# Optimization experiments

Measured on AMD Instinct MI355X. Metric: run time of the kernel, lower is better.

## Reference

```python
import jax, jax.numpy as jnp
import numpy as np
from jax import lax

B, CIN, H, W = 16, 256, 64, 64
DP = 512          # displace_planes
COUT = 256        # outplanes
NUM_OFFSET = 64   # displace_planes // BIND_CHAN(8)
K = 5             # DPOOL_SIZE (odd)
EPS = float(np.finfo(np.float32).eps)
BN_EPS = 1e-5
EXP_CLAMP = 88.722835


def conv1x1(x, w, b):
    # x: [B,C,H,W], w: [O,C], b: [O]
    return jnp.einsum('bchw,oc->bohw', x, w) + b[None, :, None, None]


def batchnorm(x, gamma, beta):
    m = x.mean(axis=(0, 2, 3))
    v = x.var(axis=(0, 2, 3))
    inv = lax.rsqrt(v + BN_EPS)
    return (x - m[None, :, None, None]) * (inv * gamma)[None, :, None, None] + beta[None, :, None, None]


def dynamic_pool(x, sigma):
    # per-channel Gaussian depthwise conv in exp space, back to log space
    r = (jnp.arange(K) - K // 2).astype(jnp.float32)
    dissq = r[:, None] ** 2 + r[None, :] ** 2                     # [K,K]
    kern = jnp.exp(-(dissq / 2.0)[None] / (sigma ** 2 + EPS)[:, None, None])  # [C,K,K]
    kern = kern / kern.sum(axis=(1, 2), keepdims=True)
    expx = jnp.exp(jnp.minimum(x, EXP_CLAMP))
    out = lax.conv_general_dilated(
        expx, kern[:, None],                                      # rhs [C,1,K,K]
        window_strides=(1, 1), padding=[(K // 2, K // 2)] * 2,
        dimension_numbers=('NCHW', 'OIHW', 'NCHW'),
        feature_group_count=DP)
    return jnp.log(out + EPS)


def displace(feat, offsets):
    # feat: [B,C,H,W]; offsets: [NUM_OFFSET,2] (dy,dx), each bound to C//NUM_OFFSET channels.
    # Per-channel uniform bilinear shift with zero padding outside the map.
    Bn, C, Hn, Wn = feat.shape
    chan = C // NUM_OFFSET
    dy = jnp.repeat(offsets[:, 0], chan)  # [C]
    dx = jnp.repeat(offsets[:, 1], chan)
    y0 = jnp.floor(dy); x0 = jnp.floor(dx)
    fy = dy - y0; fx = dx - x0            # fractional parts (diff. wrt offsets)
    y0i = y0.astype(jnp.int32); x0i = x0.astype(jnp.int32)
    rows = jnp.arange(Hn); cols = jnp.arange(Wn)

    def one_chan(img, y0c, x0c, fyc, fxc):
        # img: [B,H,W]; shift is separable per row/col since offset is uniform
        def shifted(oy, ox):
            ry = rows + y0c + oy
            rx = cols + x0c + ox
            my = (ry >= 0) & (ry < Hn)
            mx = (rx >= 0) & (rx < Wn)
            g = img[:, jnp.clip(ry, 0, Hn - 1), :][:, :, jnp.clip(rx, 0, Wn - 1)]
            return g * (my[:, None] & mx[None, :]).astype(img.dtype)[None]
        return ((1 - fyc) * (1 - fxc) * shifted(0, 0)
                + (1 - fyc) * fxc * shifted(0, 1)
                + fyc * (1 - fxc) * shifted(1, 0)
                + fyc * fxc * shifted(1, 1))

    return jax.vmap(one_chan, in_axes=(1, 0, 0, 0, 0), out_axes=1)(feat, y0i, x0i, fy, fx)


def attention(x, w, b, gamma, beta):
    a = conv1x1(x, w, b)
    a = batchnorm(a, gamma, beta)
    a = jax.nn.softplus(a)
    # SpaceNormalization: normalize over spatial dims
    return a / a.sum(axis=(2, 3), keepdims=True)


def setup_inputs() -> dict:
    key = jax.random.key(0)
    ks = jax.random.split(key, 6)
    return {
        'x': jax.random.normal(ks[0], (B, CIN, H, W), jnp.float32),
        'pre_w': jax.random.normal(ks[1], (DP, CIN), jnp.float32) / np.sqrt(CIN),
        'pre_b': jnp.zeros((DP,), jnp.float32),
        'sigma': jnp.full((DP,), K / 2 / 2, jnp.float32),
        'offsets': jax.random.normal(ks[2], (NUM_OFFSET, 2), jnp.float32) * 3.0,
        'atten_w': jax.random.normal(ks[3], (DP, CIN), jnp.float32) / np.sqrt(CIN),
        'atten_b': jnp.zeros((DP,), jnp.float32),
        'atten_gamma': jnp.ones((DP,), jnp.float32),
        'atten_beta': jnp.zeros((DP,), jnp.float32),
        'post_w': jax.random.normal(ks[4], (COUT, DP), jnp.float32) / np.sqrt(DP),
        'post_b': jnp.zeros((COUT,), jnp.float32),
        'bn_gamma': jnp.ones((COUT,), jnp.float32),
        'bn_beta': jnp.zeros((COUT,), jnp.float32),
    }


def reference(x, pre_w, pre_b, sigma, offsets, atten_w, atten_b, atten_gamma,
              atten_beta, post_w, post_b, bn_gamma, bn_beta):
    out_pre = conv1x1(x, pre_w, pre_b)                 # [B,DP,H,W]
    out_pre = dynamic_pool(out_pre, sigma)
    out_dis = displace(out_pre, offsets)
    out_atten = attention(x, atten_w, atten_b, atten_gamma, atten_beta)
    out_post = conv1x1(out_atten * out_dis, post_w, post_b)  # [B,COUT,H,W]
    out_skip = x + out_post                            # inplanes==outplanes, stride=1
    return jax.nn.relu(batchnorm(out_skip, bn_gamma, bn_beta))
```

## Files before the change

### kernel.cpp

```cpp
#include <hip/hip_runtime.h>
#include <cmath>

#define NB   16
#define CINC 256
#define DPC  512
#define COUTC 256
#define HWS  4096
#define EPSF 1.1920928955078125e-07f
#define BN_EPS 1e-5f
#define EXP_CLAMP 88.722835f
#define SW 80

typedef unsigned int uint32;
typedef unsigned short ushort;
typedef __bf16 bf16x8 __attribute__((ext_vector_type(8)));
typedef float f32x4 __attribute__((ext_vector_type(4)));
typedef unsigned short ushort8 __attribute__((ext_vector_type(8)));

__device__ inline ushort f2bf(float f) {
    uint32 u = __builtin_bit_cast(uint32, f);
    u += 0x7fffu + ((u >> 16) & 1u);
    return (ushort)(u >> 16);
}
__device__ inline float bf2f(ushort u) {
    return __builtin_bit_cast(float, (uint32)u << 16);
}
__device__ inline float softplus_fast(float v) {
    return fmaxf(v, 0.f) + __logf(1.f + __expf(-fabsf(v)));
}
__device__ __forceinline__ void gload16(const void* g, void* l) {
    __builtin_amdgcn_global_load_lds(
        (__attribute__((address_space(1))) void*)g,
        (__attribute__((address_space(3))) void*)l, 16, 0, 0);
}

template<int OTOT, int KTOT, bool BF16_OUT, bool ADD_SKIP>
__global__ __launch_bounds__(256) void mfma_gemm_k(
    const ushort* __restrict__ A, const ushort* __restrict__ BT,
    const float* __restrict__ bias1, const float* __restrict__ bias2,
    const float* __restrict__ skip, void* __restrict__ outv) {
    const int hw0 = blockIdx.x * 128;
    const int o0  = blockIdx.y * 128;
    const int b   = blockIdx.z;
    __shared__ ushort As[128 * 32];
    __shared__ ushort Bs[128 * 32];
    const int tid  = threadIdx.x;
    const int lane = tid & 63;
    const int w    = tid >> 6;
    const int wm0  = (w >> 1) * 64;
    const int wn0  = (w & 1) * 64;

    f32x4 acc[4][4] = {};

    const ushort* Ab = A + (size_t)o0 * KTOT;
    const ushort* Bb = BT + ((size_t)b * HWS + hw0) * KTOT;
    const int rsub  = lane >> 2;
    const int ksubp = ((lane & 3) ^ ((lane >> 3) & 3)) * 8;

    for (int step = 0; step < KTOT / 32; ++step) {
        const int k0 = step * 32;
#pragma unroll
        for (int i = 0; i < 2; ++i) {
            const int row = w * 32 + i * 16 + rsub;
            gload16(Ab + (size_t)row * KTOT + k0 + ksubp, &As[(w * 32 + i * 16) * 32]);
            gload16(Bb + (size_t)row * KTOT + k0 + ksubp, &Bs[(w * 32 + i * 16) * 32]);
        }
        __syncthreads();
        bf16x8 af[4], bfr[4];
#pragma unroll
        for (int mi = 0; mi < 4; ++mi) {
            int row = wm0 + mi * 16 + (lane & 15);
            int sl = (lane >> 4) ^ ((row >> 1) & 3);
            af[mi] = *reinterpret_cast<const bf16x8*>(As + row * 32 + sl * 8);
        }
#pragma unroll
        for (int ni = 0; ni < 4; ++ni) {
            int row = wn0 + ni * 16 + (lane & 15);
            int sl = (lane >> 4) ^ ((row >> 1) & 3);
            bfr[ni] = *reinterpret_cast<const bf16x8*>(Bs + row * 32 + sl * 8);
        }
#pragma unroll
        for (int mi = 0; mi < 4; ++mi)
#pragma unroll
            for (int ni = 0; ni < 4; ++ni)
                acc[mi][ni] = __builtin_amdgcn_mfma_f32_16x16x32_bf16(af[mi], bfr[ni], acc[mi][ni], 0, 0, 0);
        __syncthreads();
    }

#pragma unroll
    for (int mi = 0; mi < 4; ++mi) {
#pragma unroll
        for (int r = 0; r < 4; ++r) {
            int o = o0 + wm0 + mi * 16 + ((lane >> 4) << 2) + r;
            float bi = (o < 512) ? bias1[o] : bias2[o - 512];
            size_t base = ((size_t)b * OTOT + o) * HWS + hw0 + wn0 + (lane & 15);
            if constexpr (BF16_OUT) {
                ushort* outp = (ushort*)outv;
#pragma unroll
                for (int ni = 0; ni < 4; ++ni)
                    outp[base + ni * 16] = f2bf(acc[mi][ni][r] + bi);
            } else {
                float* outp = (float*)outv;
#pragma unroll
                for (int ni = 0; ni < 4; ++ni) {
                    float v = acc[mi][ni][r] + bi;
                    if constexpr (ADD_SKIP) v += skip[base + ni * 16];
                    outp[base + ni * 16] = v;
                }
            }
        }
    }
}

__global__ __launch_bounds__(256) void castT_k(const float* __restrict__ x,
                                               ushort* __restrict__ xT) {
    const int b = blockIdx.z, c0 = blockIdx.y * 64, hw0 = blockIdx.x * 64;
    __shared__ float tile[64][65];
    const int tid = threadIdx.x;
#pragma unroll
    for (int r = 0; r < 16; ++r) {
        int cl = r * 4 + (tid >> 6), hwl = tid & 63;
        tile[cl][hwl] = x[((size_t)b * CINC + c0 + cl) * HWS + hw0 + hwl];
    }
    __syncthreads();
#pragma unroll
    for (int r = 0; r < 16; ++r) {
        int hwl = r * 4 + (tid >> 6), cl = tid & 63;
        xT[((size_t)b * HWS + hw0 + hwl) * CINC + c0 + cl] = f2bf(tile[cl][hwl]);
    }
}

__global__ __launch_bounds__(256) void cast_k(const float* __restrict__ in,
                                              ushort* __restrict__ out, int n) {
    int i = (blockIdx.x * 256 + threadIdx.x) * 4;
    if (i < n) {
        float4 v = *reinterpret_cast<const float4*>(in + i);
        out[i + 0] = f2bf(v.x); out[i + 1] = f2bf(v.y);
        out[i + 2] = f2bf(v.z); out[i + 3] = f2bf(v.w);
    }
}

__global__ __launch_bounds__(256) void pooldisp_k(ushort* __restrict__ dp,
                                                  const float* __restrict__ sigma,
                                                  const float* __restrict__ offsets) {
    const int bc = blockIdx.x;
    const int b = bc >> 9, c = bc & 511;
    __shared__ ushort ex[68 * SW];
    __shared__ ushort tmp[68 * SW];
    const int tid = threadIdx.x;
    ushort* ip = dp + ((size_t)b * 1024 + c) * HWS;

    float s = sigma[c];
    float inv = 0.5f / (s * s + EPSF);
    float g0 = __expf(-4.f * inv), g1 = __expf(-1.f * inv);
    float gs = g0 + g1 + 1.f + g1 + g0;
    float rnorm = 1.f / (gs * gs);

    if (tid < 168) {
        int row, colc;
        if (tid < 40) {
            row = (tid < 20) ? (tid / 10) : (66 + (tid - 20) / 10);
            colc = (tid % 10) * 8;
        } else {
            int k = tid - 40;
            row = 2 + (k >> 1);
            colc = (k & 1) ? 72 : 0;
        }
        ushort8 z = {0, 0, 0, 0, 0, 0, 0, 0};
        *reinterpret_cast<ushort8*>(&ex[row * SW + colc]) = z;
    }
#pragma unroll
    for (int t = 0; t < 2; ++t) {
        int p = (tid + t * 256) * 8;
        int h = p >> 6, w = p & 63;
        ushort8 v = *reinterpret_cast<const ushort8*>(ip + p);
        ushort8 e;
#pragma unroll
        for (int q = 0; q < 8; ++q)
            e[q] = f2bf(__expf(fminf(bf2f(v[q]), EXP_CLAMP)));
        *reinterpret_cast<ushort8*>(&ex[(h + 2) * SW + 8 + w]) = e;
    }
    __syncthreads();

    for (int t = 0; t < 3; ++t) {
        int task = tid + t * 256;
        if (task < 544) {
            int r = task >> 3, wgc = (task & 7) * 8;
            ushort8 c0 = *reinterpret_cast<const ushort8*>(&ex[r * SW + wgc]);
            ushort8 c1 = *reinterpret_cast<const ushort8*>(&ex[r * SW + wgc + 8]);
            ushort8 c2 = *reinterpret_cast<const ushort8*>(&ex[r * SW + wgc + 16]);
            float P[24];
#pragma unroll
            for (int q = 0; q < 8; ++q) {
                P[q] = bf2f(c0[q]); P[8 + q] = bf2f(c1[q]); P[16 + q] = bf2f(c2[q]);
            }
            ushort8 o;
#pragma unroll
            for (int j = 0; j < 8; ++j)
                o[j] = f2bf(g0 * (P[6 + j] + P[10 + j]) + g1 * (P[7 + j] + P[9 + j]) + P[8 + j]);
            *reinterpret_cast<ushort8*>(&tmp[r * SW + wgc + 8]) = o;
        }
    }
    __syncthreads();

#pragma unroll
    for (int t = 0; t < 2; ++t) {
        int task = tid + t * 256;
        int h = task >> 3, wgc = (task & 7) * 8;
        ushort8 t0 = *reinterpret_cast<const ushort8*>(&tmp[(h + 0) * SW + wgc + 8]);
        ushort8 t1 = *reinterpret_cast<const ushort8*>(&tmp[(h + 1) * SW + wgc + 8]);
        ushort8 t2 = *reinterpret_cast<const ushort8*>(&tmp[(h + 2) * SW + wgc + 8]);
        ushort8 t3 = *reinterpret_cast<const ushort8*>(&tmp[(h + 3) * SW + wgc + 8]);
        ushort8 t4 = *reinterpret_cast<const ushort8*>(&tmp[(h + 4) * SW + wgc + 8]);
        ushort8 o;
#pragma unroll
        for (int j = 0; j < 8; ++j) {
            float v = g0 * (bf2f(t0[j]) + bf2f(t4[j]))
                    + g1 * (bf2f(t1[j]) + bf2f(t3[j])) + bf2f(t2[j]);
            o[j] = f2bf(__logf(v * rnorm + EPSF));
        }
        *reinterpret_cast<ushort8*>(&ex[(h + 2) * SW + 8 + wgc]) = o;
    }
    __syncthreads();

    int oi = c >> 3;
    float dy = offsets[oi * 2 + 0];
    float dx = offsets[oi * 2 + 1];
    float y0f = floorf(dy), x0f = floorf(dx);
    float fy = dy - y0f, fx = dx - x0f;
    int y0 = (int)y0f, x0 = (int)x0f;
    float w00 = (1.f - fy) * (1.f - fx), w01 = (1.f - fy) * fx;
    float w10 = fy * (1.f - fx),         w11 = fy * fx;
#pragma unroll
    for (int t = 0; t < 2; ++t) {
        int p = (tid + t * 256) * 8;
        int h = p >> 6, w = p & 63;
        int ry0 = h + y0, ry1 = ry0 + 1;
        bool my0 = (ry0 >= 0) & (ry0 < 64);
        bool my1 = (ry1 >= 0) & (ry1 < 64);
        ushort8 ov;
#pragma unroll
        for (int q = 0; q < 8; ++q) {
            int rx0 = w + q + x0, rx1 = rx0 + 1;
            bool mx0 = (rx0 >= 0) & (rx0 < 64);
            bool mx1 = (rx1 >= 0) & (rx1 < 64);
            float acc = 0.f;
            if (my0 & mx0) acc += w00 * bf2f(ex[(ry0 + 2) * SW + 8 + rx0]);
            if (my0 & mx1) acc += w01 * bf2f(ex[(ry0 + 2) * SW + 8 + rx1]);
            if (my1 & mx0) acc += w10 * bf2f(ex[(ry1 + 2) * SW + 8 + rx0]);
            if (my1 & mx1) acc += w11 * bf2f(ex[(ry1 + 2) * SW + 8 + rx1]);
            ov[q] = f2bf(acc);
        }
        *reinterpret_cast<ushort8*>(ip + p) = ov;
    }
}

__global__ __launch_bounds__(1024) void attstats_k(const ushort* __restrict__ dp,
                                                   const float* __restrict__ gamma,
                                                   const float* __restrict__ beta,
                                                   float* __restrict__ scale,
                                                   float* __restrict__ shift,
                                                   float* __restrict__ rsum) {
    const int c = blockIdx.x;
    const int t = threadIdx.x;
    const int wv = t >> 6, lane = t & 63;
    const ushort* p = dp + ((size_t)wv * 1024 + 512 + c) * HWS;

    ushort8 v[8];
    float s = 0.f, s2 = 0.f;
#pragma unroll
    for (int k = 0; k < 8; ++k) {
        v[k] = *reinterpret_cast<const ushort8*>(p + lane * 8 + k * 512);
#pragma unroll
        for (int j = 0; j < 8; ++j) { float f = bf2f(v[k][j]); s += f; s2 += f * f; }
    }
#pragma unroll
    for (int off = 32; off > 0; off >>= 1) {
        s += __shfl_down(s, off, 64);
        s2 += __shfl_down(s2, off, 64);
    }
    __shared__ float t1[16], t2[16], scsh[2];
    if (lane == 0) { t1[wv] = s; t2[wv] = s2; }
    __syncthreads();
    if (t == 0) {
        float S = 0.f, S2 = 0.f;
#pragma unroll
        for (int k = 0; k < 16; ++k) { S += t1[k]; S2 += t2[k]; }
        float n = (float)(NB * HWS);
        float mean = S / n;
        float var = S2 / n - mean * mean;
        float invs = rsqrtf(var + BN_EPS);
        float sc = invs * gamma[c];
        float sh = beta[c] - mean * sc;
        scale[c] = sc; shift[c] = sh;
        scsh[0] = sc; scsh[1] = sh;
    }
    __syncthreads();
    float sc = scsh[0], sh = scsh[1];
    float ps = 0.f;
#pragma unroll
    for (int k = 0; k < 8; ++k)
#pragma unroll
        for (int j = 0; j < 8; ++j)
            ps += softplus_fast(bf2f(v[k][j]) * sc + sh);
#pragma unroll
    for (int off = 32; off > 0; off >>= 1) ps += __shfl_down(ps, off, 64);
    if (lane == 0) rsum[wv * DPC + c] = 1.f / ps;
}

__global__ __launch_bounds__(256) void attmulT_k(const ushort* __restrict__ dp,
                                                 const float* __restrict__ scale,
                                                 const float* __restrict__ shift,
                                                 const float* __restrict__ rsum,
                                                 ushort* __restrict__ mT) {
    const int b = blockIdx.z, c0 = blockIdx.y * 64, hw0 = blockIdx.x * 64;
    __shared__ float tile[64][65];
    const int tid = threadIdx.x;
#pragma unroll
    for (int r = 0; r < 16; ++r) {
        int cl = r * 4 + (tid >> 6), hwl = tid & 63;
        int c = c0 + cl;
        size_t aidx = ((size_t)b * 1024 + 512 + c) * HWS + hw0 + hwl;
        size_t didx = ((size_t)b * 1024 + c) * HWS + hw0 + hwl;
        float a = bf2f(dp[aidx]) * scale[c] + shift[c];
        float m = softplus_fast(a) * rsum[b * DPC + c] * bf2f(dp[didx]);
        tile[cl][hwl] = m;
    }
    __syncthreads();
#pragma unroll
    for (int r = 0; r < 16; ++r) {
        int hwl = r * 4 + (tid >> 6), cl = tid & 63;
        mT[((size_t)b * HWS + hw0 + hwl) * DPC + c0 + cl] = f2bf(tile[cl][hwl]);
    }
}

__global__ __launch_bounds__(1024) void bnstats_k(const float* __restrict__ a,
                                                  const float* __restrict__ gamma,
                                                  const float* __restrict__ beta,
                                                  float* __restrict__ scale,
                                                  float* __restrict__ shift) {
    const int c = blockIdx.x;
    const int t = threadIdx.x;
    const int wv = t >> 6, lane = t & 63;
    const float* p = a + ((size_t)wv * COUTC + c) * HWS;
    float s = 0.f, s2 = 0.f;
#pragma unroll
    for (int k = 0; k < 16; ++k) {
        float4 v = *reinterpret_cast<const float4*>(p + lane * 4 + k * 256);
        s += v.x + v.y + v.z + v.w;
        s2 += v.x * v.x + v.y * v.y + v.z * v.z + v.w * v.w;
    }
#pragma unroll
    for (int off = 32; off > 0; off >>= 1) {
        s += __shfl_down(s, off, 64);
        s2 += __shfl_down(s2, off, 64);
    }
    __shared__ float t1[16], t2[16];
    if (lane == 0) { t1[wv] = s; t2[wv] = s2; }
    __syncthreads();
    if (t == 0) {
        float S = 0.f, S2 = 0.f;
#pragma unroll
        for (int k = 0; k < 16; ++k) { S += t1[k]; S2 += t2[k]; }
        float n = (float)(NB * HWS);
        float mean = S / n;
        float var = S2 / n - mean * mean;
        float invs = rsqrtf(var + BN_EPS);
        float sc = invs * gamma[c];
        scale[c] = sc;
        shift[c] = beta[c] - mean * sc;
    }
}

__global__ __launch_bounds__(256) void final_k(float* __restrict__ out,
                                               const float* __restrict__ scale,
                                               const float* __restrict__ shift) {
    int i = blockIdx.x * 256 + threadIdx.x;
    int c = (i >> 12) & (COUTC - 1);
    float v = out[i] * scale[c] + shift[c];
    out[i] = fmaxf(v, 0.f);
}

extern "C" void kernel_launch(void* const* d_in, const int* in_sizes, int n_in,
                              void* d_out, int out_size, void* d_ws, size_t ws_size,
                              hipStream_t stream) {
    const float* x           = (const float*)d_in[0];
    const float* pre_w       = (const float*)d_in[1];
    const float* pre_b       = (const float*)d_in[2];
    const float* sigma       = (const float*)d_in[3];
    const float* offsets     = (const float*)d_in[4];
    const float* atten_w     = (const float*)d_in[5];
    const float* atten_b     = (const float*)d_in[6];
    const float* atten_gamma = (const float*)d_in[7];
    const float* atten_beta  = (const float*)d_in[8];
    const float* post_w      = (const float*)d_in[9];
    const float* post_b      = (const float*)d_in[10];
    const float* bn_gamma    = (const float*)d_in[11];
    const float* bn_beta     = (const float*)d_in[12];
    float* out = (float*)d_out;

    char* wsb = (char*)d_ws;
    ushort* xT    = (ushort*)(wsb);
    ushort* wbig  = (ushort*)(wsb + ((size_t)32 << 20));
    ushort* wpost = wbig + 1024 * 256;
    float*  stats = (float*)(wsb + ((size_t)33 << 20));
    ushort* dpout = (ushort*)(wsb + ((size_t)34 << 20));
    ushort* mT    = (ushort*)(wsb + ((size_t)162 << 20));

    float* scaleA = stats;
    float* shiftA = stats + 512;
    float* rsum   = stats + 1024;
    float* scale2 = stats + 9216;
    float* shift2 = stats + 9472;

    castT_k<<<dim3(64, 4, NB), 256, 0, stream>>>(x, xT);
    cast_k<<<128, 256, 0, stream>>>(pre_w,   wbig,             DPC * CINC);
    cast_k<<<128, 256, 0, stream>>>(atten_w, wbig + 512 * 256, DPC * CINC);
    cast_k<<<128, 256, 0, stream>>>(post_w,  wpost,            COUTC * DPC);

    mfma_gemm_k<1024, CINC, true, false><<<dim3(32, 8, NB), 256, 0, stream>>>(
        wbig, xT, pre_b, atten_b, nullptr, dpout);
    pooldisp_k<<<NB * DPC, 256, 0, stream>>>(dpout, sigma, offsets);
    attstats_k<<<DPC, 1024, 0, stream>>>(dpout, atten_gamma, atten_beta,
                                         scaleA, shiftA, rsum);
    attmulT_k<<<dim3(64, 8, NB), 256, 0, stream>>>(dpout, scaleA, shiftA, rsum, mT);
    mfma_gemm_k<COUTC, DPC, false, true><<<dim3(32, 2, NB), 256, 0, stream>>>(
        wpost, mT, post_b, post_b, x, out);
    bnstats_k<<<COUTC, 1024, 0, stream>>>(out, bn_gamma, bn_beta, scale2, shift2);
    final_k<<<out_size / 256, 256, 0, stream>>>(out, scale2, shift2);
}
```

Before: 305.2 us.

## Double K-step in GEMM, fuse exp+horizontal blur in pool kernel with fp32 scratch

The GEMM now loads a 64-wide K slice per barrier pair, which halves the number of __syncthreads per tile at the cost of twice the LDS. The pool/displace kernel fuses the exp and horizontal 5-tap blur into one pass that reads halo values directly from global memory, keeps the intermediate in fp32 LDS, and writes the pooled result into a separate bf16 plane. This removes one LDS pass and its barrier. The bf16 conversion switches to the compiler's native cast. The fp32 intermediate also changes rounding slightly and raises LDS use per block.

```diff
diff --git a/kernel.cpp b/kernel.cpp
--- a/kernel.cpp
+++ b/kernel.cpp
@@ -9,7 +9,8 @@
 #define EPSF 1.1920928955078125e-07f
 #define BN_EPS 1e-5f
 #define EXP_CLAMP 88.722835f
-#define SW 80
+#define TS 76
+#define PS 72
 
 typedef unsigned int uint32;
 typedef unsigned short ushort;
@@ -18,9 +19,8 @@
 typedef unsigned short ushort8 __attribute__((ext_vector_type(8)));
 
 __device__ inline ushort f2bf(float f) {
-    uint32 u = __builtin_bit_cast(uint32, f);
-    u += 0x7fffu + ((u >> 16) & 1u);
-    return (ushort)(u >> 16);
+    __bf16 h = (__bf16)f;
+    return __builtin_bit_cast(ushort, h);
 }
 __device__ inline float bf2f(ushort u) {
     return __builtin_bit_cast(float, (uint32)u << 16);
@@ -42,8 +42,8 @@
     const int hw0 = blockIdx.x * 128;
     const int o0  = blockIdx.y * 128;
     const int b   = blockIdx.z;
-    __shared__ ushort As[128 * 32];
-    __shared__ ushort Bs[128 * 32];
+    __shared__ ushort As[2 * 128 * 32];
+    __shared__ ushort Bs[2 * 128 * 32];
     const int tid  = threadIdx.x;
     const int lane = tid & 63;
     const int w    = tid >> 6;
@@ -57,33 +57,43 @@
     const int rsub  = lane >> 2;
     const int ksubp = ((lane & 3) ^ ((lane >> 3) & 3)) * 8;
 
-    for (int step = 0; step < KTOT / 32; ++step) {
-        const int k0 = step * 32;
-#pragma unroll
-        for (int i = 0; i < 2; ++i) {
-            const int row = w * 32 + i * 16 + rsub;
-            gload16(Ab + (size_t)row * KTOT + k0 + ksubp, &As[(w * 32 + i * 16) * 32]);
-            gload16(Bb + (size_t)row * KTOT + k0 + ksubp, &Bs[(w * 32 + i * 16) * 32]);
+    for (int step = 0; step < KTOT / 64; ++step) {
+        const int k0 = step * 64;
+#pragma unroll
+        for (int h = 0; h < 2; ++h)
+#pragma unroll
+            for (int i = 0; i < 2; ++i) {
+                const int row = w * 32 + i * 16 + rsub;
+                gload16(Ab + (size_t)row * KTOT + k0 + h * 32 + ksubp,
+                        &As[h * 4096 + (w * 32 + i * 16) * 32]);
+                gload16(Bb + (size_t)row * KTOT + k0 + h * 32 + ksubp,
+                        &Bs[h * 4096 + (w * 32 + i * 16) * 32]);
+            }
+        __syncthreads();
+        bf16x8 af[2][4], bfr[2][4];
+#pragma unroll
+        for (int h = 0; h < 2; ++h) {
+#pragma unroll
+            for (int mi = 0; mi < 4; ++mi) {
+                int row = wm0 + mi * 16 + (lane & 15);
+                int sl = (lane >> 4) ^ ((row >> 1) & 3);
+                af[h][mi] = *reinterpret_cast<const bf16x8*>(As + h * 4096 + row * 32 + sl * 8);
+            }
+#pragma unroll
+            for (int ni = 0; ni < 4; ++ni) {
+                int row = wn0 + ni * 16 + (lane & 15);
+                int sl = (lane >> 4) ^ ((row >> 1) & 3);
+                bfr[h][ni] = *reinterpret_cast<const bf16x8*>(Bs + h * 4096 + row * 32 + sl * 8);
+            }
         }
-        __syncthreads();
-        bf16x8 af[4], bfr[4];
-#pragma unroll
-        for (int mi = 0; mi < 4; ++mi) {
-            int row = wm0 + mi * 16 + (lane & 15);
-            int sl = (lane >> 4) ^ ((row >> 1) & 3);
-            af[mi] = *reinterpret_cast<const bf16x8*>(As + row * 32 + sl * 8);
-        }
-#pragma unroll
-        for (int ni = 0; ni < 4; ++ni) {
-            int row = wn0 + ni * 16 + (lane & 15);
-            int sl = (lane >> 4) ^ ((row >> 1) & 3);
-            bfr[ni] = *reinterpret_cast<const bf16x8*>(Bs + row * 32 + sl * 8);
-        }
-#pragma unroll
-        for (int mi = 0; mi < 4; ++mi)
-#pragma unroll
-            for (int ni = 0; ni < 4; ++ni)
-                acc[mi][ni] = __builtin_amdgcn_mfma_f32_16x16x32_bf16(af[mi], bfr[ni], acc[mi][ni], 0, 0, 0);
+#pragma unroll
+        for (int h = 0; h < 2; ++h)
+#pragma unroll
+            for (int mi = 0; mi < 4; ++mi)
+#pragma unroll
+                for (int ni = 0; ni < 4; ++ni)
+                    acc[mi][ni] = __builtin_amdgcn_mfma_f32_16x16x32_bf16(
+                        af[h][mi], bfr[h][ni], acc[mi][ni], 0, 0, 0);
         __syncthreads();
     }
 
@@ -145,8 +155,8 @@
                                                   const float* __restrict__ offsets) {
     const int bc = blockIdx.x;
     const int b = bc >> 9, c = bc & 511;
-    __shared__ ushort ex[68 * SW];
-    __shared__ ushort tmp[68 * SW];
+    __shared__ float  tmp[68 * TS];
+    __shared__ ushort pl[64 * PS];
     const int tid = threadIdx.x;
     ushort* ip = dp + ((size_t)b * 1024 + c) * HWS;
 
@@ -156,70 +166,57 @@
     float gs = g0 + g1 + 1.f + g1 + g0;
     float rnorm = 1.f / (gs * gs);
 
-    if (tid < 168) {
-        int row, colc;
-        if (tid < 40) {
-            row = (tid < 20) ? (tid / 10) : (66 + (tid - 20) / 10);
-            colc = (tid % 10) * 8;
-        } else {
-            int k = tid - 40;
-            row = 2 + (k >> 1);
-            colc = (k & 1) ? 72 : 0;
-        }
-        ushort8 z = {0, 0, 0, 0, 0, 0, 0, 0};
-        *reinterpret_cast<ushort8*>(&ex[row * SW + colc]) = z;
-    }
-#pragma unroll
-    for (int t = 0; t < 2; ++t) {
-        int p = (tid + t * 256) * 8;
-        int h = p >> 6, w = p & 63;
-        ushort8 v = *reinterpret_cast<const ushort8*>(ip + p);
-        ushort8 e;
-#pragma unroll
-        for (int q = 0; q < 8; ++q)
-            e[q] = f2bf(__expf(fminf(bf2f(v[q]), EXP_CLAMP)));
-        *reinterpret_cast<ushort8*>(&ex[(h + 2) * SW + 8 + w]) = e;
-    }
-    __syncthreads();
-
-    for (int t = 0; t < 3; ++t) {
-        int task = tid + t * 256;
-        if (task < 544) {
-            int r = task >> 3, wgc = (task & 7) * 8;
-            ushort8 c0 = *reinterpret_cast<const ushort8*>(&ex[r * SW + wgc]);
-            ushort8 c1 = *reinterpret_cast<const ushort8*>(&ex[r * SW + wgc + 8]);
-            ushort8 c2 = *reinterpret_cast<const ushort8*>(&ex[r * SW + wgc + 16]);
-            float P[24];
-#pragma unroll
-            for (int q = 0; q < 8; ++q) {
-                P[q] = bf2f(c0[q]); P[8 + q] = bf2f(c1[q]); P[16 + q] = bf2f(c2[q]);
-            }
-            ushort8 o;
-#pragma unroll
-            for (int j = 0; j < 8; ++j)
-                o[j] = f2bf(g0 * (P[6 + j] + P[10 + j]) + g1 * (P[7 + j] + P[9 + j]) + P[8 + j]);
-            *reinterpret_cast<ushort8*>(&tmp[r * SW + wgc + 8]) = o;
-        }
-    }
-    __syncthreads();
-
+    if (tid < 64) {
+        int r = tid >> 4;
+        int rr = (r < 2) ? r : 64 + r;
+        int cq = (tid & 15) * 4;
+        f32x4 z = {0.f, 0.f, 0.f, 0.f};
+        *reinterpret_cast<f32x4*>(&tmp[rr * TS + cq]) = z;
+    }
 #pragma unroll
     for (int t = 0; t < 2; ++t) {
         int task = tid + t * 256;
-        int h = task >> 3, wgc = (task & 7) * 8;
-        ushort8 t0 = *reinterpret_cast<const ushort8*>(&tmp[(h + 0) * SW + wgc + 8]);
-        ushort8 t1 = *reinterpret_cast<const ushort8*>(&tmp[(h + 1) * SW + wgc + 8]);
-        ushort8 t2 = *reinterpret_cast<const ushort8*>(&tmp[(h + 2) * SW + wgc + 8]);
-        ushort8 t3 = *reinterpret_cast<const ushort8*>(&tmp[(h + 3) * SW + wgc + 8]);
-        ushort8 t4 = *reinterpret_cast<const ushort8*>(&tmp[(h + 4) * SW + wgc + 8]);
-        ushort8 o;
-#pragma unroll
-        for (int j = 0; j < 8; ++j) {
-            float v = g0 * (bf2f(t0[j]) + bf2f(t4[j]))
-                    + g1 * (bf2f(t1[j]) + bf2f(t3[j])) + bf2f(t2[j]);
+        int hr = task >> 3, w0 = (task & 7) * 8;
+        const ushort* rp = ip + hr * 64 + w0;
+        ushort8 mv = *reinterpret_cast<const ushort8*>(rp);
+        float e[12];
+        e[0] = (w0 > 0) ? __expf(fminf(bf2f(rp[-2]), EXP_CLAMP)) : 0.f;
+        e[1] = (w0 > 0) ? __expf(fminf(bf2f(rp[-1]), EXP_CLAMP)) : 0.f;
+#pragma unroll
+        for (int q = 0; q < 8; ++q)
+            e[2 + q] = __expf(fminf(bf2f(mv[q]), EXP_CLAMP));
+        e[10] = (w0 < 56) ? __expf(fminf(bf2f(rp[8]), EXP_CLAMP)) : 0.f;
+        e[11] = (w0 < 56) ? __expf(fminf(bf2f(rp[9]), EXP_CLAMP)) : 0.f;
+        f32x4 o0, o1;
+#pragma unroll
+        for (int j = 0; j < 4; ++j) {
+            o0[j] = g0 * (e[j] + e[j + 4]) + g1 * (e[j + 1] + e[j + 3]) + e[j + 2];
+            o1[j] = g0 * (e[j + 4] + e[j + 8]) + g1 * (e[j + 5] + e[j + 7]) + e[j + 6];
+        }
+        *reinterpret_cast<f32x4*>(&tmp[(hr + 2) * TS + w0]) = o0;
+        *reinterpret_cast<f32x4*>(&tmp[(hr + 2) * TS + w0 + 4]) = o1;
+    }
+    __syncthreads();
+
+#pragma unroll
+    for (int t = 0; t < 4; ++t) {
+        int task = tid + t * 256;
+        int h = task >> 4, wq = (task & 15) * 4;
+        f32x4 t0 = *reinterpret_cast<const f32x4*>(&tmp[(h + 0) * TS + wq]);
+        f32x4 t1 = *reinterpret_cast<const f32x4*>(&tmp[(h + 1) * TS + wq]);
+        f32x4 t2 = *reinterpret_cast<const f32x4*>(&tmp[(h + 2) * TS + wq]);
+        f32x4 t3 = *reinterpret_cast<const f32x4*>(&tmp[(h + 3) * TS + wq]);
+        f32x4 t4 = *reinterpret_cast<const f32x4*>(&tmp[(h + 4) * TS + wq]);
+        ushort o[4];
+#pragma unroll
+        for (int j = 0; j < 4; ++j) {
+            float v = g0 * (t0[j] + t4[j]) + g1 * (t1[j] + t3[j]) + t2[j];
             o[j] = f2bf(__logf(v * rnorm + EPSF));
         }
-        *reinterpret_cast<ushort8*>(&ex[(h + 2) * SW + 8 + wgc]) = o;
+        *reinterpret_cast<uint32*>(&pl[h * PS + wq]) =
+            (uint32)o[0] | ((uint32)o[1] << 16);
+        *reinterpret_cast<uint32*>(&pl[h * PS + wq + 2]) =
+            (uint32)o[2] | ((uint32)o[3] << 16);
     }
     __syncthreads();
 
@@ -245,10 +242,10 @@
             bool mx0 = (rx0 >= 0) & (rx0 < 64);
             bool mx1 = (rx1 >= 0) & (rx1 < 64);
             float acc = 0.f;
-            if (my0 & mx0) acc += w00 * bf2f(ex[(ry0 + 2) * SW + 8 + rx0]);
-            if (my0 & mx1) acc += w01 * bf2f(ex[(ry0 + 2) * SW + 8 + rx1]);
-            if (my1 & mx0) acc += w10 * bf2f(ex[(ry1 + 2) * SW + 8 + rx0]);
-            if (my1 & mx1) acc += w11 * bf2f(ex[(ry1 + 2) * SW + 8 + rx1]);
+            if (my0 & mx0) acc += w00 * bf2f(pl[ry0 * PS + rx0]);
+            if (my0 & mx1) acc += w01 * bf2f(pl[ry0 * PS + rx1]);
+            if (my1 & mx0) acc += w10 * bf2f(pl[ry1 * PS + rx0]);
+            if (my1 & mx1) acc += w11 * bf2f(pl[ry1 * PS + rx1]);
             ov[q] = f2bf(acc);
         }
         *reinterpret_cast<ushort8*>(ip + p) = ov;
```

Result: faster. 297.9 us (-2.4%).
